# Kernel optimization log

Measured on AMD Instinct MI355X. Metric: run time of the kernel, lower is better.

The kernel has to match this reference:

```python
import jax, jax.numpy as jnp
import numpy as np

E, D, MULT, K = 8, 1024, 4, 2   # num_experts, hidden_dim, mlp_multiplier, top-k
B, S = 4, 2048
H = MULT * D


def setup_inputs() -> dict:
    key = jax.random.key(0)
    k0, k1, k2, k3 = jax.random.split(key, 4)
    x = jax.random.normal(k0, (B, S, D), dtype=jnp.float32)
    Wr = jax.random.normal(k1, (E, D), dtype=jnp.float32) * (D ** -0.5)        # router (no bias)
    W1 = jax.random.normal(k2, (E, D, H), dtype=jnp.float32) * (D ** -0.5)     # expert fc1
    b1 = jnp.zeros((E, H), dtype=jnp.float32)
    W2 = jax.random.normal(k3, (E, H, D), dtype=jnp.float32) * (H ** -0.5)     # expert fc2
    b2 = jnp.zeros((E, D), dtype=jnp.float32)
    return {"x": x, "Wr": Wr, "W1": W1, "b1": b1, "W2": W2, "b2": b2}


def reference(x, Wr, W1, b1, W2, b2):
    # Router: softmax over experts then top-k -> per-token combine weights.
    probs = jax.nn.softmax(jnp.einsum("bsd,ed->bse", x, Wr), axis=-1)  # [B,S,E]
    topv, topi = jax.lax.top_k(probs, K)                                # [B,S,K]
    # combine[b,s,e] = sum_k topv * 1[topi==e]  (same math as the masked scatter-add)
    combine = jnp.sum(topv[..., None] * jax.nn.one_hot(topi, E, dtype=x.dtype), axis=2)  # [B,S,E]

    def body(acc, params):
        w1, bb1, w2, bb2, ce = params  # ce: [B,S] combine weight for this expert
        h = jax.nn.gelu(jnp.einsum("bsd,dh->bsh", x, w1) + bb1, approximate=False)
        y = jnp.einsum("bsh,hd->bsd", h, w2) + bb2
        return acc + ce[..., None] * y, None

    cE = jnp.moveaxis(combine, -1, 0)  # [E,B,S]
    out, _ = jax.lax.scan(body, jnp.zeros_like(x), (W1, b1, W2, b2, cE))
    return out
```

## Files before the change

kernel.cpp:

```cpp
#include <hip/hip_runtime.h>
#include <hip/hip_bf16.h>

#define E_   8
#define D_   1024
#define H_   4096
#define T_   8192
#define TM   128
#define BK   64
#define CAP  17408
#define NBY  136
#define CK   2

typedef __attribute__((ext_vector_type(8))) short short8;
typedef __attribute__((ext_vector_type(4))) float floatx4;

__device__ __forceinline__ unsigned short f2bf(float f) {
    unsigned u = __float_as_uint(f);
    u += 0x7fffu + ((u >> 16) & 1u);
    return (unsigned short)(u >> 16);
}
__device__ __forceinline__ float bf2f(unsigned short u) {
    return __uint_as_float((unsigned)u << 16);
}

#define GLP16(g, l)                                                             \
    __builtin_amdgcn_global_load_lds((const __attribute__((address_space(1))) void*)(g), \
                                     (__attribute__((address_space(3))) void*)(l), 16, 0, 0)

__global__ __launch_bounds__(64) void router_kernel(
    const float* __restrict__ x, const float* __restrict__ Wr,
    int* __restrict__ cnt, int* __restrict__ tok_list,
    int2* __restrict__ inv_ei, float2* __restrict__ inv_w)
{
    int t = blockIdx.x;
    int lane = threadIdx.x;
    const float* xr = x + (size_t)t * D_;
    float acc[E_];
#pragma unroll
    for (int e = 0; e < E_; ++e) acc[e] = 0.f;
    for (int it = 0; it < D_ / 64; ++it) {
        float xv = xr[lane + it * 64];
#pragma unroll
        for (int e = 0; e < E_; ++e) acc[e] += xv * Wr[e * D_ + lane + it * 64];
    }
#pragma unroll
    for (int e = 0; e < E_; ++e) {
#pragma unroll
        for (int off = 32; off; off >>= 1) acc[e] += __shfl_xor(acc[e], off);
    }
    if (lane == 0) {
        float m = acc[0];
#pragma unroll
        for (int e = 1; e < E_; ++e) m = fmaxf(m, acc[e]);
        float p[E_]; float s = 0.f;
#pragma unroll
        for (int e = 0; e < E_; ++e) { p[e] = expf(acc[e] - m); s += p[e]; }
        float inv = 1.f / s;
        int i1 = 0; float v1 = p[0];
#pragma unroll
        for (int e = 1; e < E_; ++e) if (p[e] > v1) { v1 = p[e]; i1 = e; }
        int i2 = -1; float v2 = -1.f;
#pragma unroll
        for (int e = 0; e < E_; ++e) { if (e == i1) continue; if (p[e] > v2) { v2 = p[e]; i2 = e; } }
        v1 *= inv; v2 *= inv;
        int pos1 = atomicAdd(&cnt[i1], 1);
        tok_list[i1 * T_ + pos1] = t;
        int pos2 = atomicAdd(&cnt[i2], 1);
        tok_list[i2 * T_ + pos2] = t;
        inv_ei[t] = make_int2(i1 | (pos1 << 3), i2 | (pos2 << 3));
        inv_w[t] = make_float2(v1, v2);
    }
}

__global__ void offsets_kernel(const int* __restrict__ cnt, int* __restrict__ start)
{
    if (threadIdx.x == 0) {
        int s = 0;
        for (int e = 0; e < E_; ++e) {
            start[e] = s;
            s += (cnt[e] + TM - 1) / TM * TM;
        }
        start[E_] = s;
    }
}

__global__ __launch_bounds__(256) void gather_kernel(
    const float* __restrict__ x, const int* __restrict__ cnt, const int* __restrict__ start,
    const int* __restrict__ tok_list, unsigned short* __restrict__ xg)
{
    int row = blockIdx.x;
    int tid = threadIdx.x;
    int tot = start[E_];
    if (row >= tot) return;
    int e = 0;
    while (e < E_ - 1 && row >= start[e + 1]) ++e;
    int idx = row - start[e];
    unsigned short* dst = xg + (size_t)row * D_;
    if (idx < cnt[e]) {
        int t = tok_list[e * T_ + idx];
        const float4* src = (const float4*)(x + (size_t)t * D_);
        float4 v = src[tid];
        ushort4 o; o.x = f2bf(v.x); o.y = f2bf(v.y); o.z = f2bf(v.z); o.w = f2bf(v.w);
        ((ushort4*)dst)[tid] = o;
    } else {
        ((ushort4*)dst)[tid] = make_ushort4(0, 0, 0, 0);
    }
}

__global__ __launch_bounds__(256) void transpose_cvt(
    const float* __restrict__ in, unsigned short* __restrict__ out, int R, int C)
{
    __shared__ float tile[32][33];
    int e = blockIdx.z;
    int c0 = blockIdx.x * 32, r0 = blockIdx.y * 32;
    const float* src = in + (size_t)e * R * C;
    unsigned short* dst = out + (size_t)e * R * C;
    int tx = threadIdx.x & 31, ty = threadIdx.x >> 5;
#pragma unroll
    for (int i = 0; i < 32; i += 8)
        tile[ty + i][tx] = src[(size_t)(r0 + ty + i) * C + c0 + tx];
    __syncthreads();
#pragma unroll
    for (int i = 0; i < 32; i += 8)
        dst[(size_t)(c0 + ty + i) * R + r0 + tx] = f2bf(tile[tx][ty + i]);
}

__global__ __launch_bounds__(256) void fc1_kernel(
    const unsigned short* __restrict__ xg, const unsigned short* __restrict__ w1t,
    const float* __restrict__ b1, const int* __restrict__ start, unsigned short* __restrict__ h)
{
    __shared__ __align__(16) unsigned short Asm[TM * BK];
    __shared__ __align__(16) unsigned short Bsm[TM * BK];

    int row0 = blockIdx.y * TM;
    int tot = start[E_];
    if (row0 >= tot) return;
    int e = 0;
    while (e < E_ - 1 && row0 >= start[e + 1]) ++e;

    int n0 = blockIdx.x * TM;
    const unsigned short* Ag = xg + (size_t)row0 * D_;
    const unsigned short* Bg = w1t + (size_t)e * H_ * D_ + (size_t)n0 * D_;

    int tid = threadIdx.x;
    int wid = tid >> 6, lane = tid & 63;
    int wm = wid >> 1, wn = wid & 1;
    int quad = lane >> 4, r16 = lane & 15;
    int srow = (lane >> 3);
    int scol = ((lane & 7) ^ srow) * 8;
    int rsw = r16 & 7;

    floatx4 acc[4][4];
#pragma unroll
    for (int i = 0; i < 4; ++i)
#pragma unroll
        for (int j = 0; j < 4; ++j) acc[i][j] = (floatx4){0.f, 0.f, 0.f, 0.f};

    for (int kc = 0; kc < D_ / BK; ++kc) {
        int k0 = kc * BK;
#pragma unroll
        for (int q = 0; q < 4; ++q) {
            int rb = wid * 32 + q * 8;
            GLP16(Ag + (size_t)(rb + srow) * D_ + k0 + scol, Asm + rb * BK);
            GLP16(Bg + (size_t)(rb + srow) * D_ + k0 + scol, Bsm + rb * BK);
        }
        __syncthreads();
#pragma unroll
        for (int ks = 0; ks < 2; ++ks) {
            short8 af[4], bfr[4];
#pragma unroll
            for (int i = 0; i < 4; ++i)
                af[i] = *(const short8*)(Asm + (wm * 64 + i * 16 + r16) * BK + ((ks * 4 + quad) ^ rsw) * 8);
#pragma unroll
            for (int j = 0; j < 4; ++j)
                bfr[j] = *(const short8*)(Bsm + (wn * 64 + j * 16 + r16) * BK + ((ks * 4 + quad) ^ rsw) * 8);
#pragma unroll
            for (int i = 0; i < 4; ++i)
#pragma unroll
                for (int j = 0; j < 4; ++j)
                    acc[i][j] = __builtin_amdgcn_mfma_f32_16x16x32_bf16(af[i], bfr[j], acc[i][j], 0, 0, 0);
        }
        __syncthreads();
    }

    const float* b1e = b1 + (size_t)e * H_;
    float bj[4];
#pragma unroll
    for (int j = 0; j < 4; ++j) bj[j] = b1e[n0 + wn * 64 + j * 16 + r16];
#pragma unroll
    for (int i = 0; i < 4; ++i) {
#pragma unroll
        for (int r = 0; r < 4; ++r) {
            size_t rowg = (size_t)row0 + wm * 64 + i * 16 + quad * 4 + r;
            unsigned short* hp = h + rowg * H_ + n0 + wn * 64 + r16;
#pragma unroll
            for (int j = 0; j < 4; ++j) {
                float v = acc[i][j][r] + bj[j];
                float u = 1.5957691f * v * fmaf(0.044715f, v * v, 1.f);
                float g = v * __builtin_amdgcn_rcpf(1.f + __expf(-u));
                hp[j * 16] = f2bf(g);
            }
        }
    }
}

__global__ __launch_bounds__(256) void fc2_kernel(
    const unsigned short* __restrict__ h, const unsigned short* __restrict__ w2t,
    const int* __restrict__ start, unsigned short* __restrict__ y)
{
    __shared__ __align__(16) unsigned short Asm[TM * BK];
    __shared__ __align__(16) unsigned short Bsm[TM * BK];

    int row0 = blockIdx.y * TM;
    int tot = start[E_];
    if (row0 >= tot) return;
    int e = 0;
    while (e < E_ - 1 && row0 >= start[e + 1]) ++e;

    int n0 = blockIdx.x * TM;
    const unsigned short* Ag = h + (size_t)row0 * H_;
    const unsigned short* Bg = w2t + (size_t)e * D_ * H_ + (size_t)n0 * H_;

    int tid = threadIdx.x;
    int wid = tid >> 6, lane = tid & 63;
    int wm = wid >> 1, wn = wid & 1;
    int quad = lane >> 4, r16 = lane & 15;
    int srow = (lane >> 3);
    int scol = ((lane & 7) ^ srow) * 8;
    int rsw = r16 & 7;

    floatx4 acc[4][4];
#pragma unroll
    for (int i = 0; i < 4; ++i)
#pragma unroll
        for (int j = 0; j < 4; ++j) acc[i][j] = (floatx4){0.f, 0.f, 0.f, 0.f};

    const int KITERS = H_ / BK / CK;
    int kbase = blockIdx.z * KITERS;
    for (int kc = kbase; kc < kbase + KITERS; ++kc) {
        int k0 = kc * BK;
#pragma unroll
        for (int q = 0; q < 4; ++q) {
            int rb = wid * 32 + q * 8;
            GLP16(Ag + (size_t)(rb + srow) * H_ + k0 + scol, Asm + rb * BK);
            GLP16(Bg + (size_t)(rb + srow) * H_ + k0 + scol, Bsm + rb * BK);
        }
        __syncthreads();
#pragma unroll
        for (int ks = 0; ks < 2; ++ks) {
            short8 af[4], bfr[4];
#pragma unroll
            for (int i = 0; i < 4; ++i)
                af[i] = *(const short8*)(Asm + (wm * 64 + i * 16 + r16) * BK + ((ks * 4 + quad) ^ rsw) * 8);
#pragma unroll
            for (int j = 0; j < 4; ++j)
                bfr[j] = *(const short8*)(Bsm + (wn * 64 + j * 16 + r16) * BK + ((ks * 4 + quad) ^ rsw) * 8);
#pragma unroll
            for (int i = 0; i < 4; ++i)
#pragma unroll
                for (int j = 0; j < 4; ++j)
                    acc[i][j] = __builtin_amdgcn_mfma_f32_16x16x32_bf16(af[i], bfr[j], acc[i][j], 0, 0, 0);
        }
        __syncthreads();
    }

    unsigned short* ys = y + (size_t)blockIdx.z * CAP * D_;
#pragma unroll
    for (int i = 0; i < 4; ++i) {
#pragma unroll
        for (int r = 0; r < 4; ++r) {
            int row = row0 + wm * 64 + i * 16 + quad * 4 + r;
            unsigned short* op = ys + (size_t)row * D_ + n0 + wn * 64 + r16;
#pragma unroll
            for (int j = 0; j < 4; ++j)
                op[j * 16] = f2bf(acc[i][j][r]);
        }
    }
}

__global__ __launch_bounds__(256) void combine_kernel(
    const unsigned short* __restrict__ y, const int* __restrict__ start,
    const int2* __restrict__ inv_ei, const float2* __restrict__ inv_w,
    const float* __restrict__ b2, float* __restrict__ out)
{
    int t = blockIdx.x;
    int tid = threadIdx.x;
    int2 ei = inv_ei[t];
    float2 w = inv_w[t];
    int e1 = ei.x & 7, x1 = ei.x >> 3;
    int e2 = ei.y & 7, x2 = ei.y >> 3;
    size_t r1 = (size_t)start[e1] + x1;
    size_t r2 = (size_t)start[e2] + x2;
    const size_t SL = (size_t)CAP * D_;
    ushort4 a0 = ((const ushort4*)(y + r1 * D_))[tid];
    ushort4 a1 = ((const ushort4*)(y + SL + r1 * D_))[tid];
    ushort4 c0 = ((const ushort4*)(y + r2 * D_))[tid];
    ushort4 c1 = ((const ushort4*)(y + SL + r2 * D_))[tid];
    float4 bA = ((const float4*)(b2 + (size_t)e1 * D_))[tid];
    float4 bB = ((const float4*)(b2 + (size_t)e2 * D_))[tid];
    float4 o;
    o.x = w.x * (bf2f(a0.x) + bf2f(a1.x) + bA.x) + w.y * (bf2f(c0.x) + bf2f(c1.x) + bB.x);
    o.y = w.x * (bf2f(a0.y) + bf2f(a1.y) + bA.y) + w.y * (bf2f(c0.y) + bf2f(c1.y) + bB.y);
    o.z = w.x * (bf2f(a0.z) + bf2f(a1.z) + bA.z) + w.y * (bf2f(c0.z) + bf2f(c1.z) + bB.z);
    o.w = w.x * (bf2f(a0.w) + bf2f(a1.w) + bA.w) + w.y * (bf2f(c0.w) + bf2f(c1.w) + bB.w);
    ((float4*)(out + (size_t)t * D_))[tid] = o;
}

extern "C" void kernel_launch(void* const* d_in, const int* in_sizes, int n_in,
                              void* d_out, int out_size, void* d_ws, size_t ws_size,
                              hipStream_t stream)
{
    const float* x  = (const float*)d_in[0];
    const float* Wr = (const float*)d_in[1];
    const float* W1 = (const float*)d_in[2];
    const float* b1 = (const float*)d_in[3];
    const float* W2 = (const float*)d_in[4];
    const float* b2 = (const float*)d_in[5];
    float* out = (float*)d_out;

    char* ws = (char*)d_ws;
    int*    cnt      = (int*)ws;
    int*    start    = (int*)(ws + 64);
    int*    tok_list = (int*)(ws + 256);
    int2*   inv_ei   = (int2*)(ws + 393216);
    float2* inv_w    = (float2*)(ws + 458752);
    char* p0 = ws + (1u << 20);
    unsigned short* xg  = (unsigned short*)p0;
    unsigned short* w1t = (unsigned short*)(p0 + 35651584ull);
    unsigned short* h   = (unsigned short*)(p0 + 35651584ull + 67108864ull);
    unsigned short* w2t = (unsigned short*)(p0 + 35651584ull + 67108864ull + 142606336ull);
    unsigned short* y   = (unsigned short*)p0;
    (void)ws_size; (void)in_sizes; (void)n_in; (void)out_size;

    hipMemsetAsync(ws, 0, 64, stream);

    transpose_cvt<<<dim3(H_ / 32, D_ / 32, E_), 256, 0, stream>>>(W1, w1t, D_, H_);
    transpose_cvt<<<dim3(D_ / 32, H_ / 32, E_), 256, 0, stream>>>(W2, w2t, H_, D_);
    router_kernel<<<T_, 64, 0, stream>>>(x, Wr, cnt, tok_list, inv_ei, inv_w);
    offsets_kernel<<<1, 64, 0, stream>>>(cnt, start);
    gather_kernel<<<CAP, 256, 0, stream>>>(x, cnt, start, tok_list, xg);
    fc1_kernel<<<dim3(H_ / TM, NBY), 256, 0, stream>>>(xg, w1t, b1, start, h);
    fc2_kernel<<<dim3(D_ / TM, NBY, CK), 256, 0, stream>>>(h, w2t, start, y);
    combine_kernel<<<T_, 256, 0, stream>>>(y, start, inv_ei, inv_w, b2, out);
}
```

Before: 971.4 us.

## Widen GEMM tiles to 128x256 with 8 waves, fuse transposes, vectorize router

The fc1 and fc2 GEMMs move from 128x128 tiles with 4 waves to 128x256 tiles with 8 waves. This raises reuse of each A tile and halves the number of blocks, and fc2 now folds its K-split into blockIdx.x. The two weight transpose-and-convert launches become one kernel with 64x64 tiles, float4 loads and ushort4 stores. The router handles four tokens per block using float4 loads. The larger tiles raise LDS use and give fewer blocks per CU.

```diff
diff --git a/kernel.cpp b/kernel.cpp
--- a/kernel.cpp
+++ b/kernel.cpp
@@ -5,7 +5,8 @@
 #define D_   1024
 #define H_   4096
 #define T_   8192
-#define TM   128
+#define TMM  128
+#define TNN  256
 #define BK   64
 #define CAP  17408
 #define NBY  136
@@ -27,21 +28,25 @@
     __builtin_amdgcn_global_load_lds((const __attribute__((address_space(1))) void*)(g), \
                                      (__attribute__((address_space(3))) void*)(l), 16, 0, 0)
 
-__global__ __launch_bounds__(64) void router_kernel(
+__global__ __launch_bounds__(256) void router_kernel(
     const float* __restrict__ x, const float* __restrict__ Wr,
     int* __restrict__ cnt, int* __restrict__ tok_list,
     int2* __restrict__ inv_ei, float2* __restrict__ inv_w)
 {
-    int t = blockIdx.x;
-    int lane = threadIdx.x;
-    const float* xr = x + (size_t)t * D_;
+    int t = blockIdx.x * 4 + (threadIdx.x >> 6);
+    int lane = threadIdx.x & 63;
+    const float4* xr = (const float4*)(x + (size_t)t * D_);
     float acc[E_];
 #pragma unroll
     for (int e = 0; e < E_; ++e) acc[e] = 0.f;
-    for (int it = 0; it < D_ / 64; ++it) {
-        float xv = xr[lane + it * 64];
-#pragma unroll
-        for (int e = 0; e < E_; ++e) acc[e] += xv * Wr[e * D_ + lane + it * 64];
+#pragma unroll
+    for (int it = 0; it < D_ / 256; ++it) {
+        float4 xv = xr[lane + it * 64];
+#pragma unroll
+        for (int e = 0; e < E_; ++e) {
+            float4 wv = ((const float4*)(Wr + e * D_))[lane + it * 64];
+            acc[e] += xv.x * wv.x + xv.y * wv.y + xv.z * wv.z + xv.w * wv.w;
+        }
     }
 #pragma unroll
     for (int e = 0; e < E_; ++e) {
@@ -78,7 +83,7 @@
         int s = 0;
         for (int e = 0; e < E_; ++e) {
             start[e] = s;
-            s += (cnt[e] + TM - 1) / TM * TM;
+            s += (cnt[e] + TMM - 1) / TMM * TMM;
         }
         start[E_] = s;
     }
@@ -108,45 +113,61 @@
 }
 
 __global__ __launch_bounds__(256) void transpose_cvt(
-    const float* __restrict__ in, unsigned short* __restrict__ out, int R, int C)
-{
-    __shared__ float tile[32][33];
-    int e = blockIdx.z;
-    int c0 = blockIdx.x * 32, r0 = blockIdx.y * 32;
-    const float* src = in + (size_t)e * R * C;
-    unsigned short* dst = out + (size_t)e * R * C;
-    int tx = threadIdx.x & 31, ty = threadIdx.x >> 5;
-#pragma unroll
-    for (int i = 0; i < 32; i += 8)
-        tile[ty + i][tx] = src[(size_t)(r0 + ty + i) * C + c0 + tx];
+    const float* __restrict__ W1, const float* __restrict__ W2,
+    unsigned short* __restrict__ w1t, unsigned short* __restrict__ w2t)
+{
+    __shared__ float tile[64][65];
+    int z = blockIdx.z;
+    const float* src; unsigned short* dst; int R, C, r0, c0;
+    if (z < 8) {
+        src = W1 + (size_t)z * D_ * H_;       dst = w1t + (size_t)z * D_ * H_;
+        R = D_; C = H_; r0 = blockIdx.y * 64; c0 = blockIdx.x * 64;
+    } else {
+        src = W2 + (size_t)(z - 8) * H_ * D_; dst = w2t + (size_t)(z - 8) * H_ * D_;
+        R = H_; C = D_; r0 = blockIdx.x * 64; c0 = blockIdx.y * 64;
+    }
+    int t = threadIdx.x;
+    int r = t >> 4, c4 = (t & 15) * 4;
+#pragma unroll
+    for (int p = 0; p < 4; ++p) {
+        int row = p * 16 + r;
+        float4 v = *(const float4*)(src + (size_t)(r0 + row) * C + c0 + c4);
+        tile[row][c4 + 0] = v.x; tile[row][c4 + 1] = v.y;
+        tile[row][c4 + 2] = v.z; tile[row][c4 + 3] = v.w;
+    }
     __syncthreads();
 #pragma unroll
-    for (int i = 0; i < 32; i += 8)
-        dst[(size_t)(c0 + ty + i) * R + r0 + tx] = f2bf(tile[tx][ty + i]);
-}
-
-__global__ __launch_bounds__(256) void fc1_kernel(
+    for (int p = 0; p < 4; ++p) {
+        int orow = p * 16 + r;
+        ushort4 o;
+        o.x = f2bf(tile[c4 + 0][orow]); o.y = f2bf(tile[c4 + 1][orow]);
+        o.z = f2bf(tile[c4 + 2][orow]); o.w = f2bf(tile[c4 + 3][orow]);
+        *(ushort4*)(dst + (size_t)(c0 + orow) * R + r0 + c4) = o;
+    }
+}
+
+__global__ __launch_bounds__(512) void fc1_kernel(
     const unsigned short* __restrict__ xg, const unsigned short* __restrict__ w1t,
     const float* __restrict__ b1, const int* __restrict__ start, unsigned short* __restrict__ h)
 {
-    __shared__ __align__(16) unsigned short Asm[TM * BK];
-    __shared__ __align__(16) unsigned short Bsm[TM * BK];
-
-    int row0 = blockIdx.y * TM;
+    __shared__ __align__(16) unsigned short Asm[TMM * BK];
+    __shared__ __align__(16) unsigned short Bsm[TNN * BK];
+
+    int row0 = blockIdx.y * TMM;
     int tot = start[E_];
     if (row0 >= tot) return;
     int e = 0;
     while (e < E_ - 1 && row0 >= start[e + 1]) ++e;
 
-    int n0 = blockIdx.x * TM;
+    int n0 = blockIdx.x * TNN;
     const unsigned short* Ag = xg + (size_t)row0 * D_;
     const unsigned short* Bg = w1t + (size_t)e * H_ * D_ + (size_t)n0 * D_;
 
     int tid = threadIdx.x;
     int wid = tid >> 6, lane = tid & 63;
-    int wm = wid >> 1, wn = wid & 1;
+    int wm = wid & 1, wn = wid >> 1;
     int quad = lane >> 4, r16 = lane & 15;
-    int srow = (lane >> 3);
+    int srow = lane >> 3;
     int scol = ((lane & 7) ^ srow) * 8;
     int rsw = r16 & 7;
 
@@ -159,9 +180,13 @@
     for (int kc = 0; kc < D_ / BK; ++kc) {
         int k0 = kc * BK;
 #pragma unroll
+        for (int q = 0; q < 2; ++q) {
+            int rb = wid * 16 + q * 8;
+            GLP16(Ag + (size_t)(rb + srow) * D_ + k0 + scol, Asm + rb * BK);
+        }
+#pragma unroll
         for (int q = 0; q < 4; ++q) {
             int rb = wid * 32 + q * 8;
-            GLP16(Ag + (size_t)(rb + srow) * D_ + k0 + scol, Asm + rb * BK);
             GLP16(Bg + (size_t)(rb + srow) * D_ + k0 + scol, Bsm + rb * BK);
         }
         __syncthreads();
@@ -197,35 +222,36 @@
             for (int j = 0; j < 4; ++j) {
                 float v = acc[i][j][r] + bj[j];
                 float u = 1.5957691f * v * fmaf(0.044715f, v * v, 1.f);
-                float g = v * __builtin_amdgcn_rcpf(1.f + __expf(-u));
-                hp[j * 16] = f2bf(g);
+                float gl = v * __builtin_amdgcn_rcpf(1.f + __expf(-u));
+                hp[j * 16] = f2bf(gl);
             }
         }
     }
 }
 
-__global__ __launch_bounds__(256) void fc2_kernel(
+__global__ __launch_bounds__(512) void fc2_kernel(
     const unsigned short* __restrict__ h, const unsigned short* __restrict__ w2t,
     const int* __restrict__ start, unsigned short* __restrict__ y)
 {
-    __shared__ __align__(16) unsigned short Asm[TM * BK];
-    __shared__ __align__(16) unsigned short Bsm[TM * BK];
-
-    int row0 = blockIdx.y * TM;
+    __shared__ __align__(16) unsigned short Asm[TMM * BK];
+    __shared__ __align__(16) unsigned short Bsm[TNN * BK];
+
+    int row0 = blockIdx.y * TMM;
     int tot = start[E_];
     if (row0 >= tot) return;
     int e = 0;
     while (e < E_ - 1 && row0 >= start[e + 1]) ++e;
 
-    int n0 = blockIdx.x * TM;
+    int nblk = blockIdx.x & 3, ck = blockIdx.x >> 2;
+    int n0 = nblk * TNN;
     const unsigned short* Ag = h + (size_t)row0 * H_;
     const unsigned short* Bg = w2t + (size_t)e * D_ * H_ + (size_t)n0 * H_;
 
     int tid = threadIdx.x;
     int wid = tid >> 6, lane = tid & 63;
-    int wm = wid >> 1, wn = wid & 1;
+    int wm = wid & 1, wn = wid >> 1;
     int quad = lane >> 4, r16 = lane & 15;
-    int srow = (lane >> 3);
+    int srow = lane >> 3;
     int scol = ((lane & 7) ^ srow) * 8;
     int rsw = r16 & 7;
 
@@ -236,13 +262,17 @@
         for (int j = 0; j < 4; ++j) acc[i][j] = (floatx4){0.f, 0.f, 0.f, 0.f};
 
     const int KITERS = H_ / BK / CK;
-    int kbase = blockIdx.z * KITERS;
+    int kbase = ck * KITERS;
     for (int kc = kbase; kc < kbase + KITERS; ++kc) {
         int k0 = kc * BK;
 #pragma unroll
+        for (int q = 0; q < 2; ++q) {
+            int rb = wid * 16 + q * 8;
+            GLP16(Ag + (size_t)(rb + srow) * H_ + k0 + scol, Asm + rb * BK);
+        }
+#pragma unroll
         for (int q = 0; q < 4; ++q) {
             int rb = wid * 32 + q * 8;
-            GLP16(Ag + (size_t)(rb + srow) * H_ + k0 + scol, Asm + rb * BK);
             GLP16(Bg + (size_t)(rb + srow) * H_ + k0 + scol, Bsm + rb * BK);
         }
         __syncthreads();
@@ -264,7 +294,7 @@
         __syncthreads();
     }
 
-    unsigned short* ys = y + (size_t)blockIdx.z * CAP * D_;
+    unsigned short* ys = y + (size_t)ck * CAP * D_;
 #pragma unroll
     for (int i = 0; i < 4; ++i) {
 #pragma unroll
@@ -334,12 +364,11 @@
 
     hipMemsetAsync(ws, 0, 64, stream);
 
-    transpose_cvt<<<dim3(H_ / 32, D_ / 32, E_), 256, 0, stream>>>(W1, w1t, D_, H_);
-    transpose_cvt<<<dim3(D_ / 32, H_ / 32, E_), 256, 0, stream>>>(W2, w2t, H_, D_);
-    router_kernel<<<T_, 64, 0, stream>>>(x, Wr, cnt, tok_list, inv_ei, inv_w);
+    transpose_cvt<<<dim3(64, 16, 16), 256, 0, stream>>>(W1, W2, w1t, w2t);
+    router_kernel<<<T_ / 4, 256, 0, stream>>>(x, Wr, cnt, tok_list, inv_ei, inv_w);
     offsets_kernel<<<1, 64, 0, stream>>>(cnt, start);
     gather_kernel<<<CAP, 256, 0, stream>>>(x, cnt, start, tok_list, xg);
-    fc1_kernel<<<dim3(H_ / TM, NBY), 256, 0, stream>>>(xg, w1t, b1, start, h);
-    fc2_kernel<<<dim3(D_ / TM, NBY, CK), 256, 0, stream>>>(h, w2t, start, y);
+    fc1_kernel<<<dim3(H_ / TNN, NBY), 512, 0, stream>>>(xg, w1t, b1, start, h);
+    fc2_kernel<<<dim3((D_ / TNN) * CK, NBY), 512, 0, stream>>>(h, w2t, start, y);
     combine_kernel<<<T_, 256, 0, stream>>>(y, start, inv_ei, inv_w, b2, out);
 }
```

Result: faster. 913.7 us (-5.9%).
